# Performance work log

Hardware: AMD Instinct MI355X
Metric: run time of the kernel (lower is better)

## Reference

```python
import jax, jax.numpy as jnp
import numpy as np

HF, WF = 361, 720            # full-res equiangular grid (0.5 deg)
HP, WP = 90, 180             # processor grid (scale_factor=4)
CIN, CE, COUT = 26, 48, 24   # input chans, embed dim (4*8+8+8), output chans
K, NB = 9, 6                 # DISCO kernel basis count (3x3 morlet), nnz per output pixel
L = M = 90                   # SHT lmax / mmax on processor grid
NL = 4                       # processor blocks (even: SFNO global, odd: local DISCO)


def _make_psi(Ho, Wo, Hi, Wi, rng):
    # sparse quadrature-weighted DISCO basis: for each output pixel, NB neighbor
    # columns into the (Hi,Wi) input grid and K basis values per nonzero.
    lat = np.round(np.arange(Ho) * (Hi - 1) / max(Ho - 1, 1)).astype(np.int64)
    lon = np.round(np.arange(Wo) * Wi / Wo).astype(np.int64)
    LAT, LON = np.meshgrid(lat, lon, indexing='ij')
    offs = [(0, 0), (0, 1), (0, -1), (1, 0), (-1, 0), (1, 1)][:NB]
    idx = np.stack([np.clip(LAT + dy, 0, Hi - 1) * Wi + (LON + dx) % Wi for dy, dx in offs], -1)
    idx = idx.reshape(Ho * Wo, NB)
    vals = rng.standard_normal((K, Ho * Wo, NB)).astype(np.float32)
    vals /= np.abs(vals).sum(-1, keepdims=True) + 1e-6   # 'mean' basis normalization
    return jnp.asarray(idx, jnp.int32), jnp.asarray(vals)


def _make_leg(rng):
    # Legendre-transform matrices (quadrature-weighted fwd, inverse), m<=l triangular
    mask = (np.arange(M)[None, :] <= np.arange(L)[:, None]).astype(np.float32)
    Pw = rng.standard_normal((L, M, HP)).astype(np.float32) * mask[:, :, None] / np.sqrt(HP)
    Pi = rng.standard_normal((L, M, HP)).astype(np.float32) * mask[:, :, None] / np.sqrt(L)
    return jnp.asarray(Pw), jnp.asarray(Pi)


def _interp1d(n_out, n_in, periodic):
    if periodic:
        src = np.arange(n_out) * n_in / n_out
        i0 = np.floor(src).astype(np.int64) % n_in
        i1 = (i0 + 1) % n_in
    else:
        src = np.arange(n_out) * (n_in - 1) / (n_out - 1)
        i0 = np.floor(src).astype(np.int64)
        i1 = np.minimum(i0 + 1, n_in - 1)
    w = (src - np.floor(src)).astype(np.float32)
    return jnp.asarray(i0, jnp.int32), jnp.asarray(i1, jnp.int32), jnp.asarray(w)


def disco_conv(x, idx, vals, w):
    # x [B,Ci,Pin], idx [Pout,NB] int32, vals [K,Pout,NB], w [Co,Ci,K]
    xg = x[:, :, idx]                                   # [B,Ci,Pout,NB] sparse gather
    z = jnp.einsum('kpn,bipn->bikp', vals, xg)          # [B,Ci,K,Pout]
    return jnp.einsum('oik,bikp->bop', w, z)            # [B,Co,Pout]


def sht(g, Pw):
    xf = jnp.fft.rfft(g, axis=-1)[..., :M] / WP         # [B,C,HP,M] complex
    return jnp.einsum('lmt,bctm->bclm', Pw, xf)         # [B,C,L,M]


def isht(c, Pi):
    xf = jnp.einsum('lmt,bclm->bctm', Pi, c)            # [B,C,HP,M]
    full = jnp.zeros(xf.shape[:-1] + (WP // 2 + 1,), xf.dtype).at[..., :M].set(xf)
    return jnp.fft.irfft(full * WP, n=WP, axis=-1)


def _fwd(x, enc_psi_vals, enc_w, proc_psi_vals, lw, gw, Pw, Pi, m1, m2, ls,
         lat_w, lon_w, dec_psi_vals, dec_w,
         enc_psi_idx, proc_psi_idx, dec_psi_idx, lat_i0, lat_i1, lon_i0, lon_i1):
    B = x.shape[0]
    # encoder: full-res -> processor-grid DISCO conv (fp32 block in original)
    h = disco_conv(x.reshape(B, CIN, HF * WF), enc_psi_idx, enc_psi_vals, enc_w)
    for i in range(NL):
        if i % 2 == 0:  # SFNO global block: SHT -> per-degree dhconv -> ISHT
            c = sht(h.reshape(B, CE, HP, WP), Pw)
            c = jnp.einsum('oil,bilm->bolm', gw[i // 2], c)
            dx = isht(c, Pi).reshape(B, CE, HP * WP)
        else:           # local DISCO block
            dx = disco_conv(h, proc_psi_idx, proc_psi_vals, lw[i // 2])
        # norm = identity ('none'); MLP (1x1 convs) + GELU; layer_scale; identity skip
        dx = jax.nn.gelu(jnp.einsum('hi,bip->bhp', m1[i], dx))
        dx = jnp.einsum('oh,bhp->bop', m2[i], dx)
        h = h + ls[i][None, :, None] * dx
    # decoder: bilinear resample to full res, then full-res DISCO conv
    g = h.reshape(B, CE, HP, WP)
    u = g[:, :, lat_i0, :] * (1.0 - lat_w)[None, None, :, None] \
        + g[:, :, lat_i1, :] * lat_w[None, None, :, None]
    u = u[:, :, :, lon_i0] * (1.0 - lon_w) + u[:, :, :, lon_i1] * lon_w
    y = disco_conv(u.reshape(B, CE, HF * WF), dec_psi_idx, dec_psi_vals, dec_w)
    return y.reshape(B, COUT, HF, WF)


def setup_inputs() -> dict:
    rng = np.random.default_rng(0)
    key = jax.random.key(0)
    sn = lambda *s: jnp.asarray(rng.standard_normal(s).astype(np.float32))
    x = jax.random.normal(key, (1, CIN, HF, WF), jnp.float32)
    enc_psi_idx, enc_psi_vals = _make_psi(HP, WP, HF, WF, rng)
    proc_psi_idx, proc_psi_vals = _make_psi(HP, WP, HP, WP, rng)
    dec_psi_idx, dec_psi_vals = _make_psi(HF, WF, HF, WF, rng)
    Pw, Pi = _make_leg(rng)
    lat_i0, lat_i1, lat_w = _interp1d(HF, HP, False)
    lon_i0, lon_i1, lon_w = _interp1d(WF, WP, True)
    HD = int(2.0 * CE)
    return {
        'x': x,
        'enc_psi_idx': enc_psi_idx, 'enc_psi_vals': enc_psi_vals,
        'enc_w': 0.1 * sn(CE, CIN, K),
        'proc_psi_idx': proc_psi_idx, 'proc_psi_vals': proc_psi_vals,
        'lw': 0.1 * sn(2, CE, CE, K), 'gw': 0.1 * sn(2, CE, CE, L),
        'Pw': Pw, 'Pi': Pi,
        'm1': sn(NL, HD, CE) / np.float32(np.sqrt(CE)),
        'm2': sn(NL, CE, HD) / np.float32(np.sqrt(HD)),
        'ls': 0.1 * jnp.ones((NL, CE), jnp.float32),
        'lat_i0': lat_i0, 'lat_i1': lat_i1, 'lat_w': lat_w,
        'lon_i0': lon_i0, 'lon_i1': lon_i1, 'lon_w': lon_w,
        'dec_psi_idx': dec_psi_idx, 'dec_psi_vals': dec_psi_vals,
        'dec_w': 0.1 * sn(COUT, CE, K),
    }


def reference(x, enc_psi_idx, enc_psi_vals, enc_w, proc_psi_idx, proc_psi_vals, lw, gw,
              Pw, Pi, m1, m2, ls, lat_i0, lat_i1, lat_w, lon_i0, lon_i1, lon_w,
              dec_psi_idx, dec_psi_vals, dec_w):
    return _fwd(x, enc_psi_vals, enc_w, proc_psi_vals, lw, gw, Pw, Pi, m1, m2, ls,
                lat_w, lon_w, dec_psi_vals, dec_w,
                enc_psi_idx, proc_psi_idx, dec_psi_idx, lat_i0, lat_i1, lon_i0, lon_i1)
```

## Files before the change

kernel.cpp:

```cpp
#include <hip/hip_runtime.h>
#include <math.h>

constexpr int kHF = 361, kWF = 720;
constexpr int kHP = 90,  kWP = 180;
constexpr int kCIN = 26, kCE = 48, kCOUT = 24;
constexpr int kK = 9, kNB = 6;
constexpr int kL = 90, kM = 90;
constexpr int kNL = 4, kHD = 96;
constexpr int kNP  = kHP * kWP;
constexpr int kNPF = kHF * kWF;

#ifndef M_PI
#define M_PI 3.14159265358979323846
#endif

__global__ __launch_bounds__(256) void k_prep(float2* __restrict__ fcs, float2* __restrict__ icn,
                                              const float* __restrict__ dw, float* __restrict__ dwT,
                                              const float* __restrict__ Pw, const float* __restrict__ Pi,
                                              float* __restrict__ PwT, float* __restrict__ PiT) {
    int t = blockIdx.x * 256 + threadIdx.x;
    if (t < kM * kWP) {
        int m = t / kWP, w = t % kWP;
        double th = (2.0 * M_PI / (double)kWP) * (double)(m * w);
        double c = cos(th), s = sin(th);
        fcs[w * kM + m] = make_float2((float)(c / (double)kWP), (float)(-s / (double)kWP));
        float sc = (m == 0) ? 1.0f : 2.0f;
        icn[m * kWP + w] = make_float2(sc * (float)c, sc * (float)s);
    }
    if (t < kCOUT * kCE * kK) {
        int k = t % kK;
        int i = (t / kK) % kCE;
        int o = t / (kK * kCE);
        dwT[((size_t)i * kCOUT + o) * kK + k] = dw[t];
    }
    int N = kL * kM * kHP;
    if (t < 2 * N) {
        int mode = t >= N ? 1 : 0;
        int u = mode ? t - N : t;
        int l = u / (kM * kHP);
        int r = u % (kM * kHP);
        int m = r / kHP;
        int tt = r % kHP;
        if (mode == 0) PwT[(l * kHP + tt) * kM + m] = Pw[u];
        else           PiT[(tt * kL + l) * kM + m] = Pi[u];
    }
}

template <int TCIN, int TCOUT, int OG>
__global__ __launch_bounds__(256) void k_disco(const float* __restrict__ src, int srcStride,
                                               const int* __restrict__ idx, const float* __restrict__ vals,
                                               const float* __restrict__ w, float* __restrict__ out, int np) {
    int gt = blockIdx.x * 256 + threadIdx.x;
    if (gt >= np * OG) return;
    int p = gt % np;
    int og = gt / np;
    constexpr int OC = TCOUT / OG;

    int qi[kNB];
#pragma unroll
    for (int n = 0; n < kNB; n++) qi[n] = idx[p * kNB + n];

    float vv[kK][kNB];
#pragma unroll
    for (int k = 0; k < kK; k++) {
        const float* vp = vals + ((size_t)k * np + p) * kNB;
#pragma unroll
        for (int n = 0; n < kNB; n += 2) {
            float2 v2 = *(const float2*)(vp + n);
            vv[k][n] = v2.x; vv[k][n + 1] = v2.y;
        }
    }

    float acc[OC];
#pragma unroll
    for (int o = 0; o < OC; o++) acc[o] = 0.0f;

    const float* wbase = w + (size_t)og * OC * TCIN * kK;

    for (int i = 0; i < TCIN; i++) {
        float xg[kNB];
#pragma unroll
        for (int n = 0; n < kNB; n++) xg[n] = src[i * srcStride + qi[n]];
        float z[kK];
#pragma unroll
        for (int k = 0; k < kK; k++) {
            float zz = 0.0f;
#pragma unroll
            for (int n = 0; n < kNB; n++) zz = fmaf(vv[k][n], xg[n], zz);
            z[k] = zz;
        }
#pragma unroll
        for (int o = 0; o < OC; o++) {
            const float* wp = wbase + ((size_t)o * TCIN + i) * kK;
            float s = acc[o];
#pragma unroll
            for (int k = 0; k < kK; k++) s = fmaf(wp[k], z[k], s);
            acc[o] = s;
        }
    }
#pragma unroll
    for (int o = 0; o < OC; o++) out[(size_t)(og * OC + o) * np + p] = acc[o];
}

__global__ __launch_bounds__(256) void k_rfft3(const float* __restrict__ g, const float2* __restrict__ fcs,
                                               float2* __restrict__ xc) {
    __shared__ float gs[8 * kWP];
    int t0 = blockIdx.x * 256;
    int t = t0 + threadIdx.x;
    constexpr int NPAIR = (kCE * kHP) / 2;
    int rp0 = t0 / kM;
    int rp1 = (t0 + 255) / kM;
    int r0 = 2 * rp0;
    int nrows = 2 * (rp1 - rp0 + 1);
    for (int j = threadIdx.x; j < nrows * kWP; j += 256) {
        int rr = j / kWP, w = j % kWP;
        int row = r0 + rr;
        if (row < kCE * kHP) gs[j] = g[(size_t)row * kWP + w];
    }
    __syncthreads();
    if (t >= NPAIR * kM) return;
    int m = t % kM;
    int rp = t / kM;
    const float* g0 = &gs[(2 * rp - r0) * kWP];
    const float* g1 = g0 + kWP;
    float ar0 = 0.0f, ai0 = 0.0f, ar1 = 0.0f, ai1 = 0.0f;
#pragma unroll 6
    for (int w = 0; w < kWP; w++) {
        float2 f = fcs[w * kM + m];
        float a = g0[w], b = g1[w];
        ar0 = fmaf(a, f.x, ar0); ai0 = fmaf(a, f.y, ai0);
        ar1 = fmaf(b, f.x, ar1); ai1 = fmaf(b, f.y, ai1);
    }
    xc[(size_t)(2 * rp) * kM + m]     = make_float2(ar0, ai0);
    xc[(size_t)(2 * rp + 1) * kM + m] = make_float2(ar1, ai1);
}

constexpr int kMT = 18;
__global__ __launch_bounds__(256) void k_sht_gmix2(const float* __restrict__ PwT,
                                                   const float2* __restrict__ xc,
                                                   const float* __restrict__ gwl,
                                                   float2* __restrict__ c2c) {
    __shared__ float2 cs[kCE][kMT];
    int l = blockIdx.x / 5;
    int m0 = (blockIdx.x % 5) * kMT;
    int tid = threadIdx.x;

    if (tid < 12 * kMT) {
        int ig = tid / kMT, mm = tid % kMT;
        int i = ig * 4;
        int m = m0 + mm;
        float ar0 = 0, ai0 = 0, ar1 = 0, ai1 = 0, ar2 = 0, ai2 = 0, ar3 = 0, ai3 = 0;
        const float*  pw = PwT + (size_t)l * kHP * kM + m;
        const float2* x0 = xc + (size_t)(i + 0) * kHP * kM + m;
        const float2* x1 = xc + (size_t)(i + 1) * kHP * kM + m;
        const float2* x2 = xc + (size_t)(i + 2) * kHP * kM + m;
        const float2* x3 = xc + (size_t)(i + 3) * kHP * kM + m;
#pragma unroll 3
        for (int tt = 0; tt < kHP; tt++) {
            float pv = pw[tt * kM];
            float2 a = x0[tt * kM], b = x1[tt * kM], c = x2[tt * kM], d = x3[tt * kM];
            ar0 = fmaf(pv, a.x, ar0); ai0 = fmaf(pv, a.y, ai0);
            ar1 = fmaf(pv, b.x, ar1); ai1 = fmaf(pv, b.y, ai1);
            ar2 = fmaf(pv, c.x, ar2); ai2 = fmaf(pv, c.y, ai2);
            ar3 = fmaf(pv, d.x, ar3); ai3 = fmaf(pv, d.y, ai3);
        }
        cs[i + 0][mm] = make_float2(ar0, ai0);
        cs[i + 1][mm] = make_float2(ar1, ai1);
        cs[i + 2][mm] = make_float2(ar2, ai2);
        cs[i + 3][mm] = make_float2(ar3, ai3);
    }
    __syncthreads();
    for (int j = tid; j < kCE * kMT; j += 256) {
        int o = j / kMT, mm = j % kMT;
        float ar = 0.0f, ai = 0.0f;
        const float* gv = gwl + (size_t)o * kCE * kL + l;
#pragma unroll 8
        for (int i = 0; i < kCE; i++) {
            float g = gv[(size_t)i * kL];
            float2 cv = cs[i][mm];
            ar = fmaf(g, cv.x, ar);
            ai = fmaf(g, cv.y, ai);
        }
        c2c[((size_t)o * kL + l) * kM + m0 + mm] = make_float2(ar, ai);
    }
}

constexpr int kCG = 4;
__global__ __launch_bounds__(192) void k_isht_irfft2(const float* __restrict__ PiT,
                                                     const float2* __restrict__ c2c,
                                                     const float2* __restrict__ icn,
                                                     float* __restrict__ dx) {
    __shared__ float2 xm[kCG][kM];
    int bi = blockIdx.x;
    int t = bi % kHP;
    int c0 = (bi / kHP) * kCG;
    int tid = threadIdx.x;

    if (tid < 2 * kM) {
        int m = tid % kM;
        int cp = tid / kM;
        int ca = c0 + cp * 2;
        float ar0 = 0, ai0 = 0, ar1 = 0, ai1 = 0;
        const float*  pv  = PiT + (size_t)t * kL * kM + m;
        const float2* cva = c2c + (size_t)ca * kL * kM + m;
        const float2* cvb = cva + (size_t)kL * kM;
#pragma unroll 6
        for (int l = 0; l < kL; l++) {
            float pp = pv[(size_t)l * kM];
            float2 a = cva[(size_t)l * kM];
            float2 b = cvb[(size_t)l * kM];
            ar0 = fmaf(pp, a.x, ar0); ai0 = fmaf(pp, a.y, ai0);
            ar1 = fmaf(pp, b.x, ar1); ai1 = fmaf(pp, b.y, ai1);
        }
        xm[cp * 2 + 0][m] = make_float2(ar0, ai0);
        xm[cp * 2 + 1][m] = make_float2(ar1, ai1);
    }
    __syncthreads();
    if (tid < kWP) {
        int w = tid;
        float a0 = 0, a1 = 0, a2 = 0, a3 = 0;
#pragma unroll 6
        for (int m = 0; m < kM; m++) {
            float2 f = icn[m * kWP + w];
            float2 x0 = xm[0][m], x1 = xm[1][m], x2 = xm[2][m], x3 = xm[3][m];
            a0 = fmaf(x0.x, f.x, a0); a0 = fmaf(-x0.y, f.y, a0);
            a1 = fmaf(x1.x, f.x, a1); a1 = fmaf(-x1.y, f.y, a1);
            a2 = fmaf(x2.x, f.x, a2); a2 = fmaf(-x2.y, f.y, a2);
            a3 = fmaf(x3.x, f.x, a3); a3 = fmaf(-x3.y, f.y, a3);
        }
        dx[((size_t)(c0 + 0) * kHP + t) * kWP + w] = a0;
        dx[((size_t)(c0 + 1) * kHP + t) * kWP + w] = a1;
        dx[((size_t)(c0 + 2) * kHP + t) * kWP + w] = a2;
        dx[((size_t)(c0 + 3) * kHP + t) * kWP + w] = a3;
    }
}

__device__ __forceinline__ float gelu_tanh(float x) {
    float x3 = x * x * x;
    float t = tanhf(0.7978845608028654f * (x + 0.044715f * x3));
    return 0.5f * x * (1.0f + t);
}

constexpr int kTP = 16;
__global__ __launch_bounds__(256) void k_mlp_f(const float* __restrict__ m1w, const float* __restrict__ m2w,
                                               const float* __restrict__ lsw, const float* __restrict__ dx,
                                               float* __restrict__ h) {
    __shared__ float xs[kCE][kTP];
    __shared__ float g1[kHD][kTP];
    int p0 = blockIdx.x * kTP;
    int tid = threadIdx.x;

    for (int j = tid; j < kCE * kTP; j += 256) {
        int i = j / kTP, pp = j % kTP;
        int p = p0 + pp;
        xs[i][pp] = (p < kNP) ? dx[(size_t)i * kNP + p] : 0.0f;
    }
    __syncthreads();
    for (int j = tid; j < kHD * kTP; j += 256) {
        int hh = j / kTP, pp = j % kTP;
        const float* w1 = m1w + (size_t)hh * kCE;
        float a = 0.0f;
#pragma unroll 8
        for (int i = 0; i < kCE; i++) a = fmaf(w1[i], xs[i][pp], a);
        g1[hh][pp] = gelu_tanh(a);
    }
    __syncthreads();
    for (int j = tid; j < kCE * kTP; j += 256) {
        int o = j / kTP, pp = j % kTP;
        int p = p0 + pp;
        if (p < kNP) {
            const float* w2 = m2w + (size_t)o * kHD;
            float a = 0.0f;
#pragma unroll 8
            for (int jj = 0; jj < kHD; jj++) a = fmaf(w2[jj], g1[jj][pp], a);
            size_t q = (size_t)o * kNP + p;
            h[q] = h[q] + lsw[o] * a;
        }
    }
}

__global__ __launch_bounds__(256) void k_dconv_d(const float* __restrict__ h,
                                                 const float* __restrict__ dvals,
                                                 const float* __restrict__ dwT,
                                                 const int* __restrict__ li0, const int* __restrict__ li1,
                                                 const float* __restrict__ lwt, const int* __restrict__ oi0,
                                                 const int* __restrict__ oi1, const float* __restrict__ owt,
                                                 float* __restrict__ out) {
    int p = blockIdx.x * 256 + threadIdx.x;
    if (p >= kNPF) return;
    int lat = p / kWF;
    int p_lon = p - lat * kWF;

    int i0r[3], i1r[3];
    float awr[3];
#pragma unroll
    for (int r = 0; r < 3; r++) {
        int Lr = lat - 1 + r;
        Lr = Lr < 0 ? 0 : (Lr > kHF - 1 ? kHF - 1 : Lr);
        i0r[r] = li0[Lr]; i1r[r] = li1[Lr]; awr[r] = lwt[Lr];
    }
    int F = min(i0r[0], min(i0r[1], i0r[2]));

    float wrow[3][3];
#pragma unroll
    for (int r = 0; r < 3; r++) {
        int r0 = i0r[r] - F, r1 = i1r[r] - F;
#pragma unroll
        for (int pr = 0; pr < 3; pr++) {
            float wv = 0.0f;
            if (pr == r0) wv += 1.0f - awr[r];
            if (pr == r1) wv += awr[r];
            wrow[r][pr] = wv;
        }
    }

    int o0d[3], o1d[3];
    float owd[3];
#pragma unroll
    for (int d = 0; d < 3; d++) {
        int lm = (p_lon + d - 1 + kWF) % kWF;
        o0d[d] = oi0[lm]; o1d[d] = oi1[lm]; owd[d] = owt[lm];
    }
    int G = o0d[0];
    float wcol[3][3];
#pragma unroll
    for (int d = 0; d < 3; d++) {
        int c0 = (o0d[d] - G + kWP) % kWP;
        int c1 = (o1d[d] - G + kWP) % kWP;
#pragma unroll
        for (int pc = 0; pc < 3; pc++) {
            float wv = 0.0f;
            if (pc == c0) wv += 1.0f - owd[d];
            if (pc == c1) wv += owd[d];
            wcol[d][pc] = wv;
        }
    }

    float vv[kK][kNB];
#pragma unroll
    for (int k = 0; k < kK; k++) {
        const float* vp = dvals + ((size_t)k * kNPF + p) * kNB;
#pragma unroll
        for (int n = 0; n < kNB; n += 2) {
            float2 v2 = *(const float2*)(vp + n);
            vv[k][n] = v2.x; vv[k][n + 1] = v2.y;
        }
    }

    const int RR[kNB] = {1, 1, 1, 2, 0, 2};
    const int CC[kNB] = {1, 2, 0, 1, 1, 2};
    float ck[kK][3][3];
#pragma unroll
    for (int k = 0; k < kK; k++)
#pragma unroll
        for (int pr = 0; pr < 3; pr++)
#pragma unroll
            for (int pc = 0; pc < 3; pc++) {
                float s = 0.0f;
#pragma unroll
                for (int n = 0; n < kNB; n++)
                    s = fmaf(vv[k][n], wrow[RR[n]][pr] * wcol[CC[n]][pc], s);
                ck[k][pr][pc] = s;
            }

    int ofs[3][3];
#pragma unroll
    for (int pr = 0; pr < 3; pr++) {
        int row = F + pr; row = row > kHP - 1 ? kHP - 1 : row;
#pragma unroll
        for (int pc = 0; pc < 3; pc++) {
            int col = (G + pc) % kWP;
            ofs[pr][pc] = row * kWP + col;
        }
    }

    float acc[kCOUT];
#pragma unroll
    for (int o = 0; o < kCOUT; o++) acc[o] = 0.0f;

    const float* wp = dwT;
    const float* hi = h;
#pragma unroll 2
    for (int i = 0; i < kCE; i++) {
        float hv[3][3];
#pragma unroll
        for (int pr = 0; pr < 3; pr++)
#pragma unroll
            for (int pc = 0; pc < 3; pc++)
                hv[pr][pc] = hi[ofs[pr][pc]];
        float z[kK];
#pragma unroll
        for (int k = 0; k < kK; k++) {
            float s = 0.0f;
#pragma unroll
            for (int pr = 0; pr < 3; pr++)
#pragma unroll
                for (int pc = 0; pc < 3; pc++)
                    s = fmaf(ck[k][pr][pc], hv[pr][pc], s);
            z[k] = s;
        }
#pragma unroll
        for (int o = 0; o < kCOUT; o++) {
            float s = acc[o];
#pragma unroll
            for (int k = 0; k < kK; k++) s = fmaf(wp[o * kK + k], z[k], s);
            acc[o] = s;
        }
        wp += kCOUT * kK;
        hi += kNP;
    }

#pragma unroll
    for (int o = 0; o < kCOUT; o++) out[(size_t)o * kNPF + p] = acc[o];
}

extern "C" void kernel_launch(void* const* d_in, const int* in_sizes, int n_in,
                              void* d_out, int out_size, void* d_ws, size_t ws_size,
                              hipStream_t stream) {
    const float* x         = (const float*)d_in[0];
    const int*   enc_idx   = (const int*)d_in[1];
    const float* enc_vals  = (const float*)d_in[2];
    const float* enc_w     = (const float*)d_in[3];
    const int*   proc_idx  = (const int*)d_in[4];
    const float* proc_vals = (const float*)d_in[5];
    const float* lw        = (const float*)d_in[6];
    const float* gw        = (const float*)d_in[7];
    const float* Pw        = (const float*)d_in[8];
    const float* Pi        = (const float*)d_in[9];
    const float* m1        = (const float*)d_in[10];
    const float* m2        = (const float*)d_in[11];
    const float* ls        = (const float*)d_in[12];
    const int*   li0       = (const int*)d_in[13];
    const int*   li1       = (const int*)d_in[14];
    const float* lwt       = (const float*)d_in[15];
    const int*   oi0       = (const int*)d_in[16];
    const int*   oi1       = (const int*)d_in[17];
    const float* owt       = (const float*)d_in[18];
    const int*   dec_idx   = (const int*)d_in[19];
    const float* dec_vals  = (const float*)d_in[20];
    const float* dec_w     = (const float*)d_in[21];
    float* out = (float*)d_out;
    (void)dec_idx;

    float* ws = (float*)d_ws;
    size_t off = 0;
    auto alloc = [&](size_t n) { float* p = ws + off; off += n; return p; };
    float*  h    = alloc((size_t)kCE * kNP);
    float2* xc   = (float2*)alloc((size_t)2 * kCE * kHP * kM);
    float2* c2c  = (float2*)alloc((size_t)2 * kCE * kL * kM);
    float*  dx   = alloc((size_t)kCE * kNP);
    float2* fcs  = (float2*)alloc((size_t)2 * kM * kWP);
    float2* icn  = (float2*)alloc((size_t)2 * kM * kWP);
    float*  PwT  = alloc((size_t)kL * kM * kHP);
    float*  PiT  = alloc((size_t)kL * kM * kHP);
    float*  dwT  = alloc((size_t)kCOUT * kCE * kK);
    (void)ws_size; (void)in_sizes; (void)n_in; (void)out_size;

    dim3 B(256);
    auto nb = [](long long n) { return dim3((unsigned)((n + 255) / 256)); };

    k_prep<<<nb(2LL * kL * kM * kHP), B, 0, stream>>>(fcs, icn, dec_w, dwT, Pw, Pi, PwT, PiT);

    k_disco<kCIN, kCE, 16><<<nb((long long)kNP * 16), B, 0, stream>>>(
        x, kNPF, enc_idx, enc_vals, enc_w, h, kNP);

    int nMlpBlocks = (kNP + kTP - 1) / kTP;
    for (int i = 0; i < kNL; i++) {
        if (i % 2 == 0) {
            const float* gwl = gw + (size_t)(i / 2) * kCE * kCE * kL;
            k_rfft3<<<nb((long long)(kCE * kHP / 2) * kM), B, 0, stream>>>(h, fcs, xc);
            k_sht_gmix2<<<dim3(kL * 5), B, 0, stream>>>(PwT, xc, gwl, c2c);
            k_isht_irfft2<<<dim3(kHP * (kCE / kCG)), dim3(192), 0, stream>>>(PiT, c2c, icn, dx);
        } else {
            const float* lwl = lw + (size_t)(i / 2) * kCE * kCE * kK;
            k_disco<kCE, kCE, 16><<<nb((long long)kNP * 16), B, 0, stream>>>(
                h, kNP, proc_idx, proc_vals, lwl, dx, kNP);
        }
        k_mlp_f<<<dim3(nMlpBlocks), B, 0, stream>>>(
            m1 + (size_t)i * kHD * kCE, m2 + (size_t)i * kCE * kHD, ls + (size_t)i * kCE, dx, h);
    }

    k_dconv_d<<<nb((long long)kNPF), B, 0, stream>>>(h, dec_vals, dwT,
                                                     li0, li1, lwt, oi0, oi1, owt, out);
}
```

Measured before the change: 652.8 us.

## Fuse local DISCO conv with MLP block and widen rfft to four rows

Adds a kernel that computes the local DISCO convolution for a 16-pixel tile into shared memory and then applies the MLP and residual update in the same block. This removes the dx round trip through global memory and one launch per odd block. Because other pixels still need to read the old activations, the fused kernel writes into a second (ping-pong) h buffer. The rfft kernel now handles four rows per thread instead of two to reuse each twiddle load more, at the cost of more registers and fewer threads.

```diff
diff --git a/kernel.cpp b/kernel.cpp
--- a/kernel.cpp
+++ b/kernel.cpp
@@ -102,37 +102,145 @@
     for (int o = 0; o < OC; o++) out[(size_t)(og * OC + o) * np + p] = acc[o];
 }
 
-__global__ __launch_bounds__(256) void k_rfft3(const float* __restrict__ g, const float2* __restrict__ fcs,
+__device__ __forceinline__ float gelu_tanh(float x) {
+    float x3 = x * x * x;
+    float t = tanhf(0.7978845608028654f * (x + 0.044715f * x3));
+    return 0.5f * x * (1.0f + t);
+}
+
+__global__ __launch_bounds__(256) void k_disco_mlp(const float* __restrict__ ho,
+                                                   const int* __restrict__ idx, const float* __restrict__ vals,
+                                                   const float* __restrict__ w,
+                                                   const float* __restrict__ m1w, const float* __restrict__ m2w,
+                                                   const float* __restrict__ lsw,
+                                                   float* __restrict__ hn) {
+    __shared__ float dxs[kCE][16];
+    __shared__ float g1[kHD][16];
+    int tid = threadIdx.x;
+    int pp = tid & 15;
+    int og = tid >> 4;
+    int p0 = blockIdx.x * 16;
+    int p = p0 + pp;
+    bool active = p < kNP;
+
+    {
+        constexpr int OC = 3;
+        int qi[kNB];
+        float vv[kK][kNB];
+        if (active) {
+#pragma unroll
+            for (int n = 0; n < kNB; n++) qi[n] = idx[p * kNB + n];
+#pragma unroll
+            for (int k = 0; k < kK; k++) {
+                const float* vp = vals + ((size_t)k * kNP + p) * kNB;
+#pragma unroll
+                for (int n = 0; n < kNB; n += 2) {
+                    float2 v2 = *(const float2*)(vp + n);
+                    vv[k][n] = v2.x; vv[k][n + 1] = v2.y;
+                }
+            }
+        } else {
+#pragma unroll
+            for (int n = 0; n < kNB; n++) qi[n] = 0;
+#pragma unroll
+            for (int k = 0; k < kK; k++)
+#pragma unroll
+                for (int n = 0; n < kNB; n++) vv[k][n] = 0.0f;
+        }
+
+        float acc[OC];
+#pragma unroll
+        for (int o = 0; o < OC; o++) acc[o] = 0.0f;
+
+        const float* wbase = w + (size_t)og * OC * kCE * kK;
+        for (int i = 0; i < kCE; i++) {
+            float xg[kNB];
+#pragma unroll
+            for (int n = 0; n < kNB; n++) xg[n] = ho[(size_t)i * kNP + qi[n]];
+            float z[kK];
+#pragma unroll
+            for (int k = 0; k < kK; k++) {
+                float zz = 0.0f;
+#pragma unroll
+                for (int n = 0; n < kNB; n++) zz = fmaf(vv[k][n], xg[n], zz);
+                z[k] = zz;
+            }
+#pragma unroll
+            for (int o = 0; o < OC; o++) {
+                const float* wp = wbase + ((size_t)o * kCE + i) * kK;
+                float s = acc[o];
+#pragma unroll
+                for (int k = 0; k < kK; k++) s = fmaf(wp[k], z[k], s);
+                acc[o] = s;
+            }
+        }
+#pragma unroll
+        for (int o = 0; o < OC; o++) dxs[og * 3 + o][pp] = acc[o];
+    }
+    __syncthreads();
+
+    for (int j = tid; j < kHD * 16; j += 256) {
+        int hh = j >> 4, pq = j & 15;
+        const float* w1 = m1w + (size_t)hh * kCE;
+        float a = 0.0f;
+#pragma unroll 8
+        for (int i = 0; i < kCE; i++) a = fmaf(w1[i], dxs[i][pq], a);
+        g1[hh][pq] = gelu_tanh(a);
+    }
+    __syncthreads();
+
+    for (int j = tid; j < kCE * 16; j += 256) {
+        int o = j >> 4, pq = j & 15;
+        int p2 = p0 + pq;
+        if (p2 < kNP) {
+            const float* w2 = m2w + (size_t)o * kHD;
+            float a = 0.0f;
+#pragma unroll 8
+            for (int jj = 0; jj < kHD; jj++) a = fmaf(w2[jj], g1[jj][pq], a);
+            size_t q = (size_t)o * kNP + p2;
+            hn[q] = ho[q] + lsw[o] * a;
+        }
+    }
+}
+
+__global__ __launch_bounds__(256) void k_rfft4(const float* __restrict__ g, const float2* __restrict__ fcs,
                                                float2* __restrict__ xc) {
-    __shared__ float gs[8 * kWP];
+    __shared__ float gs[16 * kWP];
+    constexpr int NQUAD = (kCE * kHP) / 4;
     int t0 = blockIdx.x * 256;
     int t = t0 + threadIdx.x;
-    constexpr int NPAIR = (kCE * kHP) / 2;
-    int rp0 = t0 / kM;
-    int rp1 = (t0 + 255) / kM;
-    int r0 = 2 * rp0;
-    int nrows = 2 * (rp1 - rp0 + 1);
+    int rq0 = t0 / kM;
+    int rq1 = (t0 + 255) / kM;
+    if (rq1 > NQUAD - 1) rq1 = NQUAD - 1;
+    int r0 = 4 * rq0;
+    int nrows = 4 * (rq1 - rq0 + 1);
     for (int j = threadIdx.x; j < nrows * kWP; j += 256) {
         int rr = j / kWP, w = j % kWP;
         int row = r0 + rr;
         if (row < kCE * kHP) gs[j] = g[(size_t)row * kWP + w];
     }
     __syncthreads();
-    if (t >= NPAIR * kM) return;
+    if (t >= NQUAD * kM) return;
     int m = t % kM;
-    int rp = t / kM;
-    const float* g0 = &gs[(2 * rp - r0) * kWP];
+    int rq = t / kM;
+    const float* g0 = &gs[(4 * rq - r0) * kWP];
     const float* g1 = g0 + kWP;
-    float ar0 = 0.0f, ai0 = 0.0f, ar1 = 0.0f, ai1 = 0.0f;
-#pragma unroll 6
+    const float* g2 = g1 + kWP;
+    const float* g3 = g2 + kWP;
+    float ar0 = 0, ai0 = 0, ar1 = 0, ai1 = 0, ar2 = 0, ai2 = 0, ar3 = 0, ai3 = 0;
+#pragma unroll 4
     for (int w = 0; w < kWP; w++) {
         float2 f = fcs[w * kM + m];
-        float a = g0[w], b = g1[w];
+        float a = g0[w], b = g1[w], c = g2[w], d = g3[w];
         ar0 = fmaf(a, f.x, ar0); ai0 = fmaf(a, f.y, ai0);
         ar1 = fmaf(b, f.x, ar1); ai1 = fmaf(b, f.y, ai1);
-    }
-    xc[(size_t)(2 * rp) * kM + m]     = make_float2(ar0, ai0);
-    xc[(size_t)(2 * rp + 1) * kM + m] = make_float2(ar1, ai1);
+        ar2 = fmaf(c, f.x, ar2); ai2 = fmaf(c, f.y, ai2);
+        ar3 = fmaf(d, f.x, ar3); ai3 = fmaf(d, f.y, ai3);
+    }
+    xc[(size_t)(4 * rq + 0) * kM + m] = make_float2(ar0, ai0);
+    xc[(size_t)(4 * rq + 1) * kM + m] = make_float2(ar1, ai1);
+    xc[(size_t)(4 * rq + 2) * kM + m] = make_float2(ar2, ai2);
+    xc[(size_t)(4 * rq + 3) * kM + m] = make_float2(ar3, ai3);
 }
 
 constexpr int kMT = 18;
@@ -233,12 +341,6 @@
         dx[((size_t)(c0 + 2) * kHP + t) * kWP + w] = a2;
         dx[((size_t)(c0 + 3) * kHP + t) * kWP + w] = a3;
     }
-}
-
-__device__ __forceinline__ float gelu_tanh(float x) {
-    float x3 = x * x * x;
-    float t = tanhf(0.7978845608028654f * (x + 0.044715f * x3));
-    return 0.5f * x * (1.0f + t);
 }
 
 constexpr int kTP = 16;
@@ -445,7 +547,8 @@
     float* ws = (float*)d_ws;
     size_t off = 0;
     auto alloc = [&](size_t n) { float* p = ws + off; off += n; return p; };
-    float*  h    = alloc((size_t)kCE * kNP);
+    float*  h0   = alloc((size_t)kCE * kNP);
+    float*  h1   = alloc((size_t)kCE * kNP);
     float2* xc   = (float2*)alloc((size_t)2 * kCE * kHP * kM);
     float2* c2c  = (float2*)alloc((size_t)2 * kCE * kL * kM);
     float*  dx   = alloc((size_t)kCE * kNP);
@@ -456,30 +559,37 @@
     float*  dwT  = alloc((size_t)kCOUT * kCE * kK);
     (void)ws_size; (void)in_sizes; (void)n_in; (void)out_size;
 
+    float* hbuf[2] = {h0, h1};
+    int cur = 0;
+
     dim3 B(256);
     auto nb = [](long long n) { return dim3((unsigned)((n + 255) / 256)); };
 
     k_prep<<<nb(2LL * kL * kM * kHP), B, 0, stream>>>(fcs, icn, dec_w, dwT, Pw, Pi, PwT, PiT);
 
     k_disco<kCIN, kCE, 16><<<nb((long long)kNP * 16), B, 0, stream>>>(
-        x, kNPF, enc_idx, enc_vals, enc_w, h, kNP);
+        x, kNPF, enc_idx, enc_vals, enc_w, hbuf[cur], kNP);
 
     int nMlpBlocks = (kNP + kTP - 1) / kTP;
     for (int i = 0; i < kNL; i++) {
         if (i % 2 == 0) {
             const float* gwl = gw + (size_t)(i / 2) * kCE * kCE * kL;
-            k_rfft3<<<nb((long long)(kCE * kHP / 2) * kM), B, 0, stream>>>(h, fcs, xc);
+            k_rfft4<<<nb((long long)(kCE * kHP / 4) * kM), B, 0, stream>>>(hbuf[cur], fcs, xc);
             k_sht_gmix2<<<dim3(kL * 5), B, 0, stream>>>(PwT, xc, gwl, c2c);
             k_isht_irfft2<<<dim3(kHP * (kCE / kCG)), dim3(192), 0, stream>>>(PiT, c2c, icn, dx);
+            k_mlp_f<<<dim3(nMlpBlocks), B, 0, stream>>>(
+                m1 + (size_t)i * kHD * kCE, m2 + (size_t)i * kCE * kHD, ls + (size_t)i * kCE,
+                dx, hbuf[cur]);
         } else {
             const float* lwl = lw + (size_t)(i / 2) * kCE * kCE * kK;
-            k_disco<kCE, kCE, 16><<<nb((long long)kNP * 16), B, 0, stream>>>(
-                h, kNP, proc_idx, proc_vals, lwl, dx, kNP);
-        }
-        k_mlp_f<<<dim3(nMlpBlocks), B, 0, stream>>>(
-            m1 + (size_t)i * kHD * kCE, m2 + (size_t)i * kCE * kHD, ls + (size_t)i * kCE, dx, h);
-    }
-
-    k_dconv_d<<<nb((long long)kNPF), B, 0, stream>>>(h, dec_vals, dwT,
+            k_disco_mlp<<<dim3((kNP + 15) / 16), B, 0, stream>>>(
+                hbuf[cur], proc_idx, proc_vals, lwl,
+                m1 + (size_t)i * kHD * kCE, m2 + (size_t)i * kCE * kHD, ls + (size_t)i * kCE,
+                hbuf[1 - cur]);
+            cur = 1 - cur;
+        }
+    }
+
+    k_dconv_d<<<nb((long long)kNPF), B, 0, stream>>>(hbuf[cur], dec_vals, dwT,
                                                      li0, li1, lwt, oi0, oi1, owt, out);
 }
```

Result: faster. 635.0 us, median of 2 (-2.7%).
